# Kernel tuning notes

Hardware: AMD Instinct MI355X
Metric: run time of the kernel (lower is better)

Reference implementation:

```python
import jax, jax.numpy as jnp
import numpy as np

H_HEADS = 32
KV_HEADS = 8
HEAD_DIM = 64  # hidden // num_heads = 2048 // 32


def setup_inputs() -> dict:
    key = jax.random.key(0)
    ks = jax.random.split(key, 5)
    B, T, hidden = 2, 2048, 2048
    kv_dim = KV_HEADS * HEAD_DIM
    s = 0.02
    return {
        "x": jax.random.normal(ks[0], (B, T, hidden), dtype=jnp.float32),
        "Wq": jax.random.normal(ks[1], (hidden, hidden), dtype=jnp.float32) * s,
        "Wk": jax.random.normal(ks[2], (hidden, kv_dim), dtype=jnp.float32) * s,
        "Wv": jax.random.normal(ks[3], (hidden, kv_dim), dtype=jnp.float32) * s,
        "Wo": jax.random.normal(ks[4], (hidden, hidden), dtype=jnp.float32) * s,
    }


def reference(x, Wq, Wk, Wv, Wo):
    B, T, hidden = x.shape
    h, kv, d = H_HEADS, KV_HEADS, HEAD_DIM
    g = h // kv  # GQA group size
    scale = d ** (-0.5)

    # projections
    q = (x @ Wq).reshape(B, T, h, d).transpose(0, 2, 1, 3)        # [B,h,T,d]
    k = (x @ Wk).reshape(B, T, kv, d).transpose(0, 2, 1, 3)      # [B,kv,T,d]
    v = (x @ Wv).reshape(B, T, kv, d).transpose(0, 2, 1, 3)      # [B,kv,T,d]

    # native GQA broadcast: group q heads by their shared kv head
    # (equivalent math to torch repeat_interleave on k/v)
    qg = q.reshape(B, kv, g, T, d)                                # [B,kv,g,T,d]
    scores = jnp.einsum("bkgtd,bksd->bkgts", qg, k) * scale       # [B,kv,g,T,T]
    attn = jax.nn.softmax(scores, axis=-1)
    og = jnp.einsum("bkgts,bksd->bkgtd", attn, v)                 # [B,kv,g,T,d]
    out = og.reshape(B, h, T, d).transpose(0, 2, 1, 3).reshape(B, T, h * d)
    return out @ Wo
```

## Files before the change

### kernel.cpp

```cpp
#include <hip/hip_runtime.h>

#define AS1 __attribute__((address_space(1)))
#define AS3 __attribute__((address_space(3)))

typedef unsigned short u16;
typedef unsigned int u32;
typedef __attribute__((ext_vector_type(8))) _Float16 half8;
typedef __attribute__((ext_vector_type(2))) _Float16 half2v;
typedef __attribute__((ext_vector_type(4))) u16 u16x4;
typedef __attribute__((ext_vector_type(8))) u16 u16x8;
typedef __attribute__((ext_vector_type(4))) u32 u32x4;
typedef __attribute__((ext_vector_type(4))) float f32x4;
typedef __attribute__((ext_vector_type(16))) float f32x16;

__device__ __forceinline__ u16 f2h(float f) {
    _Float16 h = (_Float16)f;
    return __builtin_bit_cast(u16, h);
}

__device__ __forceinline__ u32 pk2h(float a, float b) {
    return __builtin_bit_cast(u32, __builtin_amdgcn_cvt_pkrtz(a, b));
}

__device__ __forceinline__ float fexp2(float x) {
#if __has_builtin(__builtin_amdgcn_exp2f)
    return __builtin_amdgcn_exp2f(x);
#else
    return __expf(x * 0.69314718055994531f);
#endif
}

__device__ __forceinline__ float dot2acc(u32 w, float acc) {
#if __has_builtin(__builtin_amdgcn_fdot2)
    half2v ones = { (_Float16)1.f, (_Float16)1.f };
    return __builtin_amdgcn_fdot2(__builtin_bit_cast(half2v, w), ones, acc, false);
#else
    half2v p = __builtin_bit_cast(half2v, w);
    return acc + (float)p[0] + (float)p[1];
#endif
}

__device__ __forceinline__ void plswap(u32& a, u32& b) {
    asm("v_permlane32_swap_b32 %0, %1" : "+v"(a), "+v"(b));
}

__device__ __forceinline__ void async16(const void* g, void* l) {
    __builtin_amdgcn_global_load_lds((AS1 void*)g, (AS3 void*)l, 16, 0, 0);
}


__global__ void prep_inputs(const float* __restrict__ x, u16* __restrict__ xb,
                            const float* __restrict__ Wq, const float* __restrict__ Wk,
                            const float* __restrict__ Wv, const float* __restrict__ Wo,
                            u16* __restrict__ Wqt, u16* __restrict__ Wkvt,
                            u16* __restrict__ Wot, float qscale) {
    __shared__ float tile[32][33];
    const int z = blockIdx.z;
    if (z == 4) {
        size_t base = ((size_t)(blockIdx.y * 64 + blockIdx.x) * 256 + threadIdx.x) * 8;
        float4 v0 = *(const float4*)(x + base);
        float4 v1 = *(const float4*)(x + base + 4);
        u16x8 o = { f2h(v0.x), f2h(v0.y), f2h(v0.z), f2h(v0.w),
                    f2h(v1.x), f2h(v1.y), f2h(v1.z), f2h(v1.w) };
        *(u16x8*)(xb + base) = o;
        return;
    }
    const float* in;
    u16* out;
    int N;
    float scale = 1.f;
    if (z == 0)      { in = Wq; out = Wqt; N = 2048; scale = qscale; }
    else if (z == 1) { in = Wo; out = Wot; N = 2048; }
    else if (z == 2) { in = Wk; out = Wkvt; N = 512; }
    else             { in = Wv; out = Wkvt + (size_t)512 * 2048; N = 512; }
    const int K = 2048;
    int nb = blockIdx.x * 32, kb = blockIdx.y * 32;
    if (nb >= N) return;
    int tx = threadIdx.x & 31, ty = threadIdx.x >> 5;
#pragma unroll
    for (int r = ty; r < 32; r += 8)
        tile[r][tx] = in[(size_t)(kb + r) * N + nb + tx];
    __syncthreads();
#pragma unroll
    for (int r = ty; r < 32; r += 8)
        out[(size_t)(nb + r) * K + kb + tx] = f2h(tile[tx][r] * scale);
}


template <int OUTMODE>
__global__ __launch_bounds__(256, OUTMODE == 3 ? 3 : 2) void gemm_bt(
        const u16* __restrict__ A, const u16* __restrict__ Bt,
        void* __restrict__ C, void* __restrict__ C2,
        int M, int N, int K, int ldc) {
    __shared__ __align__(16) u16 As[2][128 * 32];
    __shared__ __align__(16) u16 Bs[2][128 * 32];
    const int m0 = blockIdx.x * 128, n0 = blockIdx.y * 128;
    const int wave = threadIdx.x >> 6, lane = threadIdx.x & 63;
    const int quad = lane >> 4, mm = lane & 15;
    const int wm = (wave >> 1) * 64, wn = (wave & 1) * 64;

    const int srow = wave * 16 + (lane >> 2);
    const int scol = 8 * ((lane & 3) ^ ((lane >> 3) & 3));

    const u16* ag0 = A + (size_t)(m0 + srow) * K + scol;
    const u16* ag1 = A + (size_t)(m0 + 64 + srow) * K + scol;
    const u16* bg0 = Bt + (size_t)(n0 + srow) * K + scol;
    const u16* bg1 = Bt + (size_t)(n0 + 64 + srow) * K + scol;
    const int soff = wave * 512 + lane * 8;

    f32x4 acc[4][4] = {};
    const int swz = (mm >> 1) & 3;

#define GST(buf)                                                              \
    {                                                                         \
        u16* ad = &As[buf][soff];                                             \
        u16* bd = &Bs[buf][soff];                                             \
        async16(ag0, ad);                                                     \
        async16(ag1, ad + 2048);                                              \
        async16(bg0, bd);                                                     \
        async16(bg1, bd + 2048);                                              \
        ag0 += 32; ag1 += 32; bg0 += 32; bg1 += 32;                           \
    }

    GST(0);
    int cur = 0;

    for (int k0 = 0; k0 < K; k0 += 32) {
        __syncthreads();
        if (k0 + 32 < K) GST(cur ^ 1);
        const u16* Ac = &As[cur][0];
        const u16* Bc = &Bs[cur][0];
        half8 af[4], bf[4];
#pragma unroll
        for (int i = 0; i < 4; i++)
            af[i] = *(const half8*)(Ac + (wm + i * 16 + mm) * 32 + (quad ^ swz) * 8);
#pragma unroll
        for (int i = 0; i < 4; i++)
            bf[i] = *(const half8*)(Bc + (wn + i * 16 + mm) * 32 + (quad ^ swz) * 8);
#pragma unroll
        for (int mi = 0; mi < 4; mi++)
#pragma unroll
            for (int ni = 0; ni < 4; ni++)
                acc[mi][ni] = __builtin_amdgcn_mfma_f32_16x16x32_f16(
                    af[mi], bf[ni], acc[mi][ni], 0, 0, 0);
        cur ^= 1;
    }
#undef GST

    if (OUTMODE == 0) {
        float* Cp = (float*)C;
#pragma unroll
        for (int mi = 0; mi < 4; mi++)
#pragma unroll
            for (int r = 0; r < 4; r++) {
                float* rp = Cp + (size_t)(m0 + wm + mi * 16 + quad * 4 + r) * ldc + n0 + wn + mm;
#pragma unroll
                for (int ni = 0; ni < 4; ni++) rp[ni * 16] = acc[mi][ni][r];
            }
    } else if (OUTMODE == 1) {
        u16* Cp = (u16*)C;
#pragma unroll
        for (int mi = 0; mi < 4; mi++)
#pragma unroll
            for (int r = 0; r < 4; r++) {
                u16* rp = Cp + (size_t)(m0 + wm + mi * 16 + quad * 4 + r) * ldc + n0 + wn + mm;
#pragma unroll
                for (int ni = 0; ni < 4; ni++) rp[ni * 16] = f2h(acc[mi][ni][r]);
            }
    } else if (OUTMODE == 2) {
        u16* Cp = (u16*)C;
#pragma unroll
        for (int mi = 0; mi < 4; mi++)
#pragma unroll
            for (int ni = 0; ni < 4; ni++) {
                int col = n0 + wn + ni * 16 + mm;
                int row0 = m0 + wm + mi * 16 + quad * 4;
                u16x4 o = { f2h(acc[mi][ni][0]), f2h(acc[mi][ni][1]),
                            f2h(acc[mi][ni][2]), f2h(acc[mi][ni][3]) };
                *(u16x4*)((u16*)Cp + (size_t)col * ldc + row0) = o;
            }
    } else {
        if (n0 < 2048) {
            u16* Qp = (u16*)C;
#pragma unroll
            for (int mi = 0; mi < 4; mi++)
#pragma unroll
                for (int r = 0; r < 4; r++) {
                    u16* rp = Qp + (size_t)(m0 + wm + mi * 16 + quad * 4 + r) * 2048 + n0 + wn + mm;
#pragma unroll
                    for (int ni = 0; ni < 4; ni++) rp[ni * 16] = f2h(acc[mi][ni][r]);
                }
        } else if (n0 < 2560) {
            u16* Kp = (u16*)C2;
#pragma unroll
            for (int mi = 0; mi < 4; mi++)
#pragma unroll
                for (int r = 0; r < 4; r++) {
                    u16* rp = Kp + (size_t)(m0 + wm + mi * 16 + quad * 4 + r) * 512 + (n0 - 2048) + wn + mm;
#pragma unroll
                    for (int ni = 0; ni < 4; ni++) rp[ni * 16] = f2h(acc[mi][ni][r]);
                }
        } else {
            u16* Vp = (u16*)C2 + (size_t)4096 * 512;
#pragma unroll
            for (int mi = 0; mi < 4; mi++)
#pragma unroll
                for (int ni = 0; ni < 4; ni++) {
                    int col = n0 - 2560 + wn + ni * 16 + mm;
                    int row0 = m0 + wm + mi * 16 + quad * 4;
                    u16x4 o = { f2h(acc[mi][ni][0]), f2h(acc[mi][ni][1]),
                                f2h(acc[mi][ni][2]), f2h(acc[mi][ni][3]) };
                    *(u16x4*)(Vp + (size_t)col * 4096 + row0) = o;
                }
        }
    }
}


template <int SPLIT>
__global__ __launch_bounds__(512, 4) void attn_fwd(const u16* __restrict__ Qb,
                                                   const u16* __restrict__ Kb,
                                                   const u16* __restrict__ Vtb,
                                                   u16* __restrict__ Ob,
                                                   float* __restrict__ Of0,
                                                   float* __restrict__ Of1,
                                                   float* __restrict__ Lf) {
    __shared__ __align__(16) u16 Ks[2][64 * 64];
    __shared__ __align__(16) u16 Vs[2][64 * 64];

    const int qtb = blockIdx.x, head = blockIdx.y;
    const int b = blockIdx.z & 1, sp = blockIdx.z >> 1;
    const int kvh = head >> 2;
    const int wave = threadIdx.x >> 6, lane = threadIdx.x & 63;
    const int h = lane >> 5;
    const int q32 = lane & 31;
    const int t = threadIdx.x;

    const size_t qrow0 = (size_t)b * 2048 + qtb * 256 + wave * 32;
    const int s_beg = sp * (2048 / SPLIT), s_end = s_beg + 2048 / SPLIT;

    half8 qf[4];
#pragma unroll
    for (int s = 0; s < 4; s++)
        qf[s] = *(const half8*)(Qb + (qrow0 + q32) * 2048 + head * 64 + s * 16 + h * 8);

    f32x16 accO[2] = {};
    float lpq[4] = {0.f, 0.f, 0.f, 0.f};

    f32x16 NEG10;
#pragma unroll
    for (int i = 0; i < 16; i++) NEG10[i] = -10.f;

    const int srow = t >> 3;
    const int lch = (t & 7) ^ (srow & 7);
    const u16* kg = Kb + ((size_t)b * 2048 + srow) * 512 + kvh * 64 + lch * 8;
    const u16* vg = Vtb + ((size_t)kvh * 64 + srow) * 4096 + b * 2048 + lch * 8;

#define STAGE(buf, s0)                                                        \
    {                                                                         \
        async16(kg + (size_t)(s0) * 512, &Ks[buf][t * 8]);                    \
        async16(vg + (s0), &Vs[buf][t * 8]);                                  \
    }

    int cur = 0;
    STAGE(0, s_beg);

    const int r0 = q32, r1 = 32 + q32;
    const int sw0 = (r0 & 7), sw1 = (r1 & 7);

    for (int s0 = s_beg; s0 < s_end; s0 += 64) {
        __syncthreads();
        int sn = s0 + 64;
        if (sn < s_end) STAGE(cur ^ 1, sn);

        const u16* Kc = &Ks[cur][0];
        const u16* Vc = &Vs[cur][0];
        const u16* Kr0 = Kc + r0 * 64;
        const u16* Kr1 = Kc + r1 * 64;

        f32x16 a0, a1;
        __builtin_amdgcn_s_setprio(1);
        {
            half8 k0 = *(const half8*)(Kr0 + ((h ^ sw0) << 3));
            a0 = __builtin_amdgcn_mfma_f32_32x32x16_f16(k0, qf[0], NEG10, 0, 0, 0);
            half8 k1 = *(const half8*)(Kr1 + ((h ^ sw1) << 3));
            a1 = __builtin_amdgcn_mfma_f32_32x32x16_f16(k1, qf[0], NEG10, 0, 0, 0);
        }
#pragma unroll
        for (int s = 1; s < 4; s++) {
            half8 k0 = *(const half8*)(Kr0 + (((2 * s + h) ^ sw0) << 3));
            a0 = __builtin_amdgcn_mfma_f32_32x32x16_f16(k0, qf[s], a0, 0, 0, 0);
            half8 k1 = *(const half8*)(Kr1 + (((2 * s + h) ^ sw1) << 3));
            a1 = __builtin_amdgcn_mfma_f32_32x32x16_f16(k1, qf[s], a1, 0, 0, 0);
        }
        __builtin_amdgcn_s_setprio(0);

        u32 w0[8];
#pragma unroll
        for (int m = 0; m < 8; m++) {
            w0[m] = pk2h(fexp2(a0[2 * m]), fexp2(a0[2 * m + 1]));
            lpq[m & 3] = dot2acc(w0[m], lpq[m & 3]);
        }

        __builtin_amdgcn_s_setprio(1);
#pragma unroll
        for (int k1 = 0; k1 < 2; k1++) {
            const int ks = k1;
            u32 d0 = w0[4 * k1 + 0], d2 = w0[4 * k1 + 2];
            u32 d1 = w0[4 * k1 + 1], d3 = w0[4 * k1 + 3];
            plswap(d0, d2);
            plswap(d1, d3);
            u32x4 pd = { d0, d1, d2, d3 };
            half8 pf = __builtin_bit_cast(half8, pd);
#pragma unroll
            for (int dt = 0; dt < 2; dt++) {
                const int rv = dt * 32 + q32;
                half8 vf = *(const half8*)(&Vc[rv * 64 + (((2 * ks + h) ^ (rv & 7)) << 3)]);
                accO[dt] = __builtin_amdgcn_mfma_f32_32x32x16_f16(vf, pf, accO[dt], 0, 0, 0);
            }
        }
        __builtin_amdgcn_s_setprio(0);

        u32 w1[8];
#pragma unroll
        for (int m = 0; m < 8; m++) {
            w1[m] = pk2h(fexp2(a1[2 * m]), fexp2(a1[2 * m + 1]));
            lpq[m & 3] = dot2acc(w1[m], lpq[m & 3]);
        }

        __builtin_amdgcn_s_setprio(1);
#pragma unroll
        for (int k1 = 0; k1 < 2; k1++) {
            const int ks = 2 + k1;
            u32 d0 = w1[4 * k1 + 0], d2 = w1[4 * k1 + 2];
            u32 d1 = w1[4 * k1 + 1], d3 = w1[4 * k1 + 3];
            plswap(d0, d2);
            plswap(d1, d3);
            u32x4 pd = { d0, d1, d2, d3 };
            half8 pf = __builtin_bit_cast(half8, pd);
#pragma unroll
            for (int dt = 0; dt < 2; dt++) {
                const int rv = dt * 32 + q32;
                half8 vf = *(const half8*)(&Vc[rv * 64 + (((2 * ks + h) ^ (rv & 7)) << 3)]);
                accO[dt] = __builtin_amdgcn_mfma_f32_32x32x16_f16(vf, pf, accO[dt], 0, 0, 0);
            }
        }
        __builtin_amdgcn_s_setprio(0);

        cur ^= 1;
    }
#undef STAGE

    float l = (lpq[0] + lpq[1]) + (lpq[2] + lpq[3]);
    l += __shfl_xor(l, 32);

    const size_t token = qrow0 + q32;
    if (SPLIT == 1) {
        float inv = 1.f / l;
#pragma unroll
        for (int dt = 0; dt < 2; dt++)
#pragma unroll
            for (int rq = 0; rq < 4; rq++) {
                u16x4 o = { f2h(accO[dt][4 * rq + 0] * inv), f2h(accO[dt][4 * rq + 1] * inv),
                            f2h(accO[dt][4 * rq + 2] * inv), f2h(accO[dt][4 * rq + 3] * inv) };
                *(u16x4*)(Ob + token * 2048 + head * 64 + dt * 32 + rq * 8 + h * 4) = o;
            }
    } else {
        float* Op = sp ? Of1 : Of0;
#pragma unroll
        for (int dt = 0; dt < 2; dt++)
#pragma unroll
            for (int rq = 0; rq < 4; rq++) {
                f32x4 o = { accO[dt][4 * rq + 0], accO[dt][4 * rq + 1],
                            accO[dt][4 * rq + 2], accO[dt][4 * rq + 3] };
                *(f32x4*)(Op + token * 2048 + head * 64 + dt * 32 + rq * 8 + h * 4) = o;
            }
        if (!h) Lf[((size_t)sp * 4096 + token) * 32 + head] = l;
    }
}


extern "C" void kernel_launch(void* const* d_in, const int* in_sizes, int n_in,
                              void* d_out, int out_size, void* d_ws, size_t ws_size,
                              hipStream_t stream) {
    (void)in_sizes; (void)n_in; (void)out_size; (void)ws_size;
    const float* x  = (const float*)d_in[0];
    const float* Wq = (const float*)d_in[1];
    const float* Wk = (const float*)d_in[2];
    const float* Wv = (const float*)d_in[3];
    const float* Wo = (const float*)d_in[4];
    float* out = (float*)d_out;

    u16* ws = (u16*)d_ws;
    u16* xb   = ws;
    u16* Wqt  = xb   + (size_t)4096 * 2048;
    u16* Wkvt = Wqt  + (size_t)2048 * 2048;
    u16* Wot  = Wkvt + (size_t)1024 * 2048;
    u16* Qb   = Wot  + (size_t)2048 * 2048;
    u16* Kb   = Qb   + (size_t)4096 * 2048;
    u16* Vtb  = Kb   + (size_t)4096 * 512;
    u16* Ob   = Vtb  + (size_t)512 * 4096;

    const float qscale = 0.125f * 1.4426950408889634f;

    prep_inputs<<<dim3(64, 64, 5), 256, 0, stream>>>(x, xb, Wq, Wk, Wv, Wo,
                                                     Wqt, Wkvt, Wot, qscale);

    gemm_bt<3><<<dim3(32, 24), 256, 0, stream>>>(xb, Wqt, Qb, Kb, 4096, 3072, 2048, 2048);

    attn_fwd<1><<<dim3(8, 32, 2), 512, 0, stream>>>(Qb, Kb, Vtb, Ob,
                                                    nullptr, nullptr, nullptr);

    gemm_bt<0><<<dim3(32, 16), 256, 0, stream>>>(Ob, Wot, out, nullptr, 4096, 2048, 2048, 2048);
}
```

Before: 315.6 us.

## Split attention KV range across two blocks with combine kernel; swizzle GEMM blocks

```diff
diff --git a/kernel.cpp b/kernel.cpp
--- a/kernel.cpp
+++ b/kernel.cpp
@@ -94,7 +94,12 @@
         int M, int N, int K, int ldc) {
     __shared__ __align__(16) u16 As[2][128 * 32];
     __shared__ __align__(16) u16 Bs[2][128 * 32];
-    const int m0 = blockIdx.x * 128, n0 = blockIdx.y * 128;
+    const int bid = blockIdx.y * gridDim.x + blockIdx.x;
+    const int cpx = (gridDim.x * gridDim.y) >> 3;
+    const int swzid = (bid & 7) * cpx + (bid >> 3);
+    const int bx = swzid % gridDim.x, by = swzid / gridDim.x;
+
+    const int m0 = bx * 128, n0 = by * 128;
     const int wave = threadIdx.x >> 6, lane = threadIdx.x & 63;
     const int quad = lane >> 4, mm = lane & 15;
     const int wm = (wave >> 1) * 64, wn = (wave & 1) * 64;
@@ -218,7 +223,7 @@
 
 
 template <int SPLIT>
-__global__ __launch_bounds__(512, 4) void attn_fwd(const u16* __restrict__ Qb,
+__global__ __launch_bounds__(512, 8) void attn_fwd(const u16* __restrict__ Qb,
                                                    const u16* __restrict__ Kb,
                                                    const u16* __restrict__ Vtb,
                                                    u16* __restrict__ Ob,
@@ -379,11 +384,25 @@
     }
 }
 
+__global__ void attn_combine(const float* __restrict__ Of0, const float* __restrict__ Of1,
+                             const float* __restrict__ Lf, u16* __restrict__ Ob) {
+    size_t idx = (size_t)blockIdx.x * 256 + threadIdx.x;
+    size_t token = idx >> 9;
+    int dq = (int)(idx & 511) * 4;
+    int head = dq >> 6;
+    float inv = 1.f / (Lf[token * 32 + head] + Lf[(4096 + token) * 32 + head]);
+    float4 a = *(const float4*)(Of0 + token * 2048 + dq);
+    float4 c = *(const float4*)(Of1 + token * 2048 + dq);
+    u16x4 o = { f2h((a.x + c.x) * inv), f2h((a.y + c.y) * inv),
+                f2h((a.z + c.z) * inv), f2h((a.w + c.w) * inv) };
+    *(u16x4*)(Ob + token * 2048 + dq) = o;
+}
+
 
 extern "C" void kernel_launch(void* const* d_in, const int* in_sizes, int n_in,
                               void* d_out, int out_size, void* d_ws, size_t ws_size,
                               hipStream_t stream) {
-    (void)in_sizes; (void)n_in; (void)out_size; (void)ws_size;
+    (void)in_sizes; (void)n_in; (void)out_size;
     const float* x  = (const float*)d_in[0];
     const float* Wq = (const float*)d_in[1];
     const float* Wk = (const float*)d_in[2];
@@ -400,6 +419,11 @@
     u16* Kb   = Qb   + (size_t)4096 * 2048;
     u16* Vtb  = Kb   + (size_t)4096 * 512;
     u16* Ob   = Vtb  + (size_t)512 * 4096;
+    u16* wend = Ob   + (size_t)4096 * 2048;
+    float* Of1 = (float*)wend;
+    float* Lf  = (float*)((char*)Of1 + (size_t)4096 * 2048 * 4);
+    size_t need = (size_t)((char*)Lf - (char*)d_ws) + (size_t)2 * 4096 * 32 * 4;
+    const bool split = ws_size >= need;
 
     const float qscale = 0.125f * 1.4426950408889634f;
 
@@ -408,8 +432,13 @@
 
     gemm_bt<3><<<dim3(32, 24), 256, 0, stream>>>(xb, Wqt, Qb, Kb, 4096, 3072, 2048, 2048);
 
-    attn_fwd<1><<<dim3(8, 32, 2), 512, 0, stream>>>(Qb, Kb, Vtb, Ob,
-                                                    nullptr, nullptr, nullptr);
+    if (split) {
+        attn_fwd<2><<<dim3(8, 32, 4), 512, 0, stream>>>(Qb, Kb, Vtb, Ob, out, Of1, Lf);
+        attn_combine<<<8192, 256, 0, stream>>>(out, Of1, Lf, Ob);
+    } else {
+        attn_fwd<1><<<dim3(8, 32, 2), 512, 0, stream>>>(Qb, Kb, Vtb, Ob,
+                                                        nullptr, nullptr, nullptr);
+    }
 
     gemm_bt<0><<<dim3(32, 16), 256, 0, stream>>>(Ob, Wot, out, nullptr, 4096, 2048, 2048, 2048);
 }
```

After: 847.3 us. +168.5%, slower.
